# Kernel tuning notes

Hardware: AMD Instinct MI355X
Metric: run time of the kernel (lower is better)

The kernel has to match this reference:

```python
import jax, jax.numpy as jnp
import numpy as np

VOCAB = 50257   # N_max = len(word_to_idx)
IN_DIM = 256
HID = 13        # forced: out Linear in_features = 2*hidden_dim must equal dec output 2*13
L = 2048


def _lstm_dir(seq, Wih, Whh, b, reverse):
    """Single-direction LSTM over seq [T, F] with zero init. b = b_ih + b_hh.
    Torch gate order: i, f, g, o."""
    H = Whh.shape[1]

    def step(carry, x_t):
        h, c = carry
        z = Wih @ x_t + Whh @ h + b                  # (4H,)
        i, f, g, o = jnp.split(z, 4)
        c2 = jax.nn.sigmoid(f) * c + jax.nn.sigmoid(i) * jnp.tanh(g)
        h2 = jax.nn.sigmoid(o) * jnp.tanh(c2)
        return (h2, c2), h2

    init = (jnp.zeros((H,), seq.dtype), jnp.zeros((H,), seq.dtype))
    (hn, cn), hs = jax.lax.scan(step, init, seq, reverse=reverse)
    return hs, hn, cn


def _dec_cell(x_scalar, h, c, Wih, Whh, b):
    """One LSTM cell step with scalar input (input_size=1). Returns new h."""
    z = Wih[:, 0] * x_scalar + Whh @ h + b
    i, f, g, o = jnp.split(z, 4)
    c2 = jax.nn.sigmoid(f) * c + jax.nn.sigmoid(i) * jnp.tanh(g)
    return jax.nn.sigmoid(o) * jnp.tanh(c2)


def setup_inputs() -> dict:
    key = jax.random.key(0)
    ks = jax.random.split(key, 16)
    s = 0.05
    G = 4 * HID  # 52; also num_layers*2*HID = 52 (proj in_features)
    return {
        "x": jax.random.randint(ks[0], (L,), 0, VOCAB),
        "emb_W": jax.random.normal(ks[1], (VOCAB + 1, IN_DIM)) * s,
        "enc_Wih0": jax.random.normal(ks[2], (2, G, IN_DIM)) * s,   # [dir, 4H, in]
        "enc_Whh0": jax.random.normal(ks[3], (2, G, HID)) * s,
        "enc_b0": jax.random.normal(ks[4], (2, G)) * s,
        "enc_Wih1": jax.random.normal(ks[5], (2, G, 2 * HID)) * s,  # layer1 input = 2*HID
        "enc_Whh1": jax.random.normal(ks[6], (2, G, HID)) * s,
        "enc_b1": jax.random.normal(ks[7], (2, G)) * s,
        "proj1_W": jax.random.normal(ks[8], (2 * HID, 2 * 2 * HID)) * s,
        "proj1_b": jax.random.normal(ks[9], (2 * HID,)) * s,
        "proj2_W": jax.random.normal(ks[10], (2 * HID, 2 * 2 * HID)) * s,
        "proj2_b": jax.random.normal(ks[11], (2 * HID,)) * s,
        "dec_Wih": jax.random.normal(ks[12], (2, G, 1)) * s,
        "dec_Whh": jax.random.normal(ks[13], (2, G, HID)) * s,
        "dec_b": jax.random.normal(ks[14], (2, G)) * s,
        "out_W": jax.random.normal(ks[15], (VOCAB, 2 * HID)) * s,
        "out_b": jnp.zeros((VOCAB,), jnp.float32),
    }


def reference(x, emb_W, enc_Wih0, enc_Whh0, enc_b0, enc_Wih1, enc_Whh1, enc_b1,
              proj1_W, proj1_b, proj2_W, proj2_b, dec_Wih, dec_Whh, dec_b,
              out_W, out_b):
    embs = emb_W[x]                                            # (L, IN_DIM)

    # Encoder: 2-layer bidirectional LSTM, batch=1 (vectors).
    hs_f0, hnf0, cnf0 = _lstm_dir(embs, enc_Wih0[0], enc_Whh0[0], enc_b0[0], False)
    hs_b0, hnb0, cnb0 = _lstm_dir(embs, enc_Wih0[1], enc_Whh0[1], enc_b0[1], True)
    out0 = jnp.concatenate([hs_f0, hs_b0], axis=-1)            # (L, 2*HID)
    _, hnf1, cnf1 = _lstm_dir(out0, enc_Wih1[0], enc_Whh1[0], enc_b1[0], False)
    _, hnb1, cnb1 = _lstm_dir(out0, enc_Wih1[1], enc_Whh1[1], enc_b1[1], True)

    # torch h_n layout: [l0_fwd, l0_bwd, l1_fwd, l1_bwd]
    h_flat = jnp.concatenate([hnf0, hnb0, hnf1, hnb1])         # (52,)
    c_flat = jnp.concatenate([cnf0, cnb0, cnf1, cnb1])
    state_h = (proj1_W @ h_flat + proj1_b).reshape(2, HID)     # dec (dir, HID) init
    state_c = (proj2_W @ c_flat + proj2_b).reshape(2, HID)

    # Decoder step 0: input -1.0 with projected initial state.
    start = jnp.float32(-1.0)
    step0 = jnp.concatenate([
        _dec_cell(start, state_h[0], state_c[0], dec_Wih[0], dec_Whh[0], dec_b[0]),
        _dec_cell(start, state_h[1], state_c[1], dec_Wih[1], dec_Whh[1], dec_b[1]),
    ])                                                          # (26,)

    # Steps i>0: original code calls self.dec(input) with NO hidden state, so each
    # step uses zero initial state and depends only on x[i-1] -> fully parallel.
    xs = x[:-1].astype(jnp.float32)                             # (L-1,)
    z0 = jnp.zeros((HID,), jnp.float32)
    rest = jax.vmap(lambda v: jnp.concatenate([
        _dec_cell(v, z0, z0, dec_Wih[0], dec_Whh[0], dec_b[0]),
        _dec_cell(v, z0, z0, dec_Wih[1], dec_Whh[1], dec_b[1]),
    ]))(xs)                                                     # (L-1, 26)

    dec_out = jnp.concatenate([step0[None, :], rest], axis=0)   # (L, 26)
    preds = dec_out @ out_W.T + out_b                           # (L, VOCAB)
    return preds, embs
```

## Files before the change

kernel.cpp:

```cpp
#include <hip/hip_runtime.h>
#include <hip/hip_bf16.h>
#include <cstdint>
#include <cstddef>

#define L      2048
#define IN_DIM 256
#define HID    13
#define G      52
#define VOCAB  50257
#define PRED_N ((size_t)L * VOOCAB)
#define L2E    1.4426950408889634f
#define INV2L2E 0.34657359027997264f
#define NTX    99
#define NTY    16
#define NTILE  (NTX * NTY)
#define GB     254
#undef PRED_N
#define PRED_N ((size_t)L * VOCAB)

static __device__ __forceinline__ float fexp2(float x) { return __builtin_amdgcn_exp2f(x); }
static __device__ __forceinline__ float frcp(float x) { return __builtin_amdgcn_rcpf(x); }
static __device__ __forceinline__ float sigm(float z) { return 1.f - frcp(fexp2(z * L2E) + 1.f); }
static __device__ __forceinline__ float tanh_(float z) { return 1.f - 2.f * frcp(fexp2(z * (2.f * L2E)) + 1.f); }
static __device__ __forceinline__ float bcast(float v, int l) {
    return __int_as_float(__builtin_amdgcn_readlane(__float_as_int(v), l));
}

__global__ void __launch_bounds__(160) k_emb_u0(
    const int* __restrict__ x, const float* __restrict__ embW,
    const float* __restrict__ Wih0, const float* __restrict__ b0,
    const float* __restrict__ dWih, const float* __restrict__ db,
    float* __restrict__ out_embs, float* __restrict__ u0, float* __restrict__ dec)
{
    __shared__ float se[IN_DIM];
    int t = blockIdx.x;
    int tid = threadIdx.x;
    if (tid < 128) {
        int rowx = x[t];
        float2 e = ((const float2*)(embW + (size_t)rowx * IN_DIM))[tid];
        se[2 * tid]     = e.x;
        se[2 * tid + 1] = e.y;
        ((float2*)(out_embs + (size_t)t * IN_DIM))[tid] = e;
    }
    __syncthreads();
    if (tid < 2 * G) {
        int dirg = tid / G, g = tid % G;
        int gate = g / HID, row = g % HID;
        float msc = (gate == 2) ? 2.f * L2E : L2E;
        float acc = b0[dirg * G + g];
        const float* w = Wih0 + (size_t)(dirg * G + g) * IN_DIM;
        #pragma unroll 8
        for (int k = 0; k < IN_DIM; ++k)
            acc = fmaf(w[k], se[k], acc);
        u0[((size_t)dirg * L + t) * 64 + gate * 16 + row] = msc * acc;
    } else if (tid < 128) {
        int p = tid - 2 * G;
        int dirp = p / 12, pp = p % 12;
        int gate = pp / 3, row = HID + pp % 3;
        u0[((size_t)dirp * L + t) * 64 + gate * 16 + row] = 0.f;
    } else if (tid < 128 + 2 * HID && t >= 1) {
        int j = tid - 128;
        int dir = j / HID, jj = j % HID;
        float v = (float)x[t - 1];
        int base = dir * G;
        float zi = fmaf(dWih[base + jj],           v, db[base + jj]);
        float zg = fmaf(dWih[base + 2 * HID + jj], v, db[base + 2 * HID + jj]);
        float zo = fmaf(dWih[base + 3 * HID + jj], v, db[base + 3 * HID + jj]);
        float c2 = sigm(zi) * tanh_(zg);
        dec[(size_t)t * (2 * HID) + j] = sigm(zo) * tanh_(c2);
    }
}

template<bool DOUT>
static __device__ __forceinline__ void chain_run(
    const float* __restrict__ ub, int pstep,
    const float* __restrict__ whh, float kcv, float onev,
    bool m16, bool m32,
    float* __restrict__ outp,
    float& hout, float& cout)
{
    float h = 0.f, c = 0.f;
    float cur[8], nxt[8];
    #pragma unroll
    for (int k = 0; k < 8; ++k) cur[k] = ub[k * pstep];
    #pragma unroll
    for (int k = 0; k < 8; ++k) nxt[k] = cur[k];
    const float* upf = ub + (ptrdiff_t)8 * pstep;

    for (int tcb = 0; tcb < L; tcb += 8) {
        if (tcb + 8 < L) {
            #pragma unroll
            for (int k = 0; k < 8; ++k) nxt[k] = upf[k * pstep];
            upf += (ptrdiff_t)8 * pstep;
        }
        #pragma unroll
        for (int k = 0; k < 8; ++k) {
            float h0 = bcast(h, 0), h1 = bcast(h, 1), h2 = bcast(h, 2), h3 = bcast(h, 3);
            float h4 = bcast(h, 4), h5 = bcast(h, 5), h6 = bcast(h, 6), h7 = bcast(h, 7);
            float h8 = bcast(h, 8), h9 = bcast(h, 9), h10 = bcast(h, 10), h11 = bcast(h, 11);
            float h12 = bcast(h, 12);
            float A = fmaf(whh[0], h0, cur[k]);
            float B = whh[1] * h1;
            float C = whh[2] * h2;
            float D = whh[3] * h3;
            A = fmaf(whh[4], h4, A);   B = fmaf(whh[5], h5, B);
            C = fmaf(whh[6], h6, C);   D = fmaf(whh[7], h7, D);
            A = fmaf(whh[8], h8, A);   B = fmaf(whh[9], h9, B);
            C = fmaf(whh[10], h10, C); D = fmaf(whh[11], h11, D);
            A = fmaf(whh[12], h12, A);
            float z = (A + B) + (C + D);
            float act = fmaf(-kcv, frcp(fexp2(z) + 1.f), onev);
            float pa = act, pb = act;
            asm("s_nop 1\n\tv_permlane16_swap_b32 %0, %1" : "+v"(pa), "+v"(pb));
            float sf = m16 ? pa : pb;
            float qa = act, qb = act;
            asm("s_nop 1\n\tv_permlane32_swap_b32 %0, %1" : "+v"(qa), "+v"(qb));
            float tg = m32 ? qa : qb;
            float ra = tg, rb = tg;
            asm("s_nop 1\n\tv_permlane16_swap_b32 %0, %1" : "+v"(ra), "+v"(rb));
            float so = m16 ? ra : rb;
            float c2 = fmaf(sf, c, act * tg);
            float th = fmaf(-2.f, frcp(fexp2(c2) + 1.f), 1.f);
            h = so * th;
            c = c2;
            if (DOUT) { *outp = h; outp += pstep; }
        }
        #pragma unroll
        for (int k = 0; k < 8; ++k) cur[k] = nxt[k];
    }
    hout = h; cout = c;
}

static __device__ __forceinline__ void chain_setup_and_run(
    const float* __restrict__ u, const float* __restrict__ Whh,
    float* __restrict__ out0p, float* __restrict__ finh, float* __restrict__ finc,
    int chain_base, int do_out0, int dir, int lane)
{
    int lg16 = lane & 15, gate = lane >> 4;
    int rsrc = gate * HID + (lg16 < HID ? lg16 : HID - 1);
    float kcv, onev;
    if (gate == 2)      { kcv = 2.f;        onev = 1.f; }
    else if (gate == 0) { kcv = 2.f * L2E;  onev = 2.f * L2E; }
    else                { kcv = 1.f;        onev = 1.f; }
    float msc = (gate == 2) ? 2.f * L2E : L2E;
    float whh[HID];
    #pragma unroll
    for (int k = 0; k < HID; ++k) whh[k] = msc * Whh[(dir * G + rsrc) * HID + k];

    int ia = lane, ib = lane;
    asm("s_nop 1\n\tv_permlane16_swap_b32 %0, %1" : "+v"(ia), "+v"(ib));
    bool m16 = (ia == (lane ^ 16));
    int ja = lane, jb = lane;
    asm("s_nop 1\n\tv_permlane32_swap_b32 %0, %1" : "+v"(ja), "+v"(jb));
    bool m32 = (ja == (lane ^ 32));

    const float* ub = u + (size_t)dir * L * 64 + (dir ? (size_t)(L - 1) * 64 : 0) + lane;
    int pstep = dir ? -64 : 64;
    float* outp = out0p + ((size_t)dir * L + (dir ? L - 1 : 0)) * 64 + lane;

    float h, c;
    if (do_out0) chain_run<true >(ub, pstep, whh, kcv, onev, m16, m32, outp, h, c);
    else         chain_run<false>(ub, pstep, whh, kcv, onev, m16, m32, outp, h, c);

    if (lane < HID) {
        finh[(chain_base + dir) * HID + lane] = h;
        finc[(chain_base + dir) * HID + lane] = c * INV2L2E;
    }
}

__global__ void __launch_bounds__(256) k_phase0(
    const float* __restrict__ u, const float* __restrict__ Whh,
    float* __restrict__ out0p, float* __restrict__ finh, float* __restrict__ finc,
    const float* __restrict__ dec, const float* __restrict__ outW,
    const float* __restrict__ outb, float* __restrict__ preds)
{
    __shared__ float sd[128][28];
    int bid = blockIdx.x;
    int tid = threadIdx.x;
    if (bid >= 2) {
        __builtin_amdgcn_s_setprio(0);
        int b = bid - 2;
        const int q = NTILE / GB, r = NTILE % GB;
        int start = b * q + (b < r ? b : r);
        int cnt   = q + (b < r ? 1 : 0);
        for (int tt = 0; tt < cnt; ++tt) {
            int tile = start + tt;
            int ix = tile % NTX, iy = tile / NTX;
            int nbase = ix * 512, i0 = iy * 128;
            __syncthreads();
            for (int li = tid; li < 128 * 26; li += 256) {
                int rr_ = li / 26, cc = li % 26;
                sd[rr_][cc] = dec[(size_t)(i0 + rr_) * 26 + cc];
            }
            __syncthreads();
            int n0 = nbase + tid, n1 = nbase + 256 + tid;
            bool a0 = n0 < VOCAB, a1 = n1 < VOCAB;
            float w0[26], w1[26], b0v = 0.f, b1v = 0.f;
            #pragma unroll
            for (int k = 0; k < 26; ++k) { w0[k] = 0.f; w1[k] = 0.f; }
            if (a0) { const float* w = outW + (size_t)n0 * 26;
                #pragma unroll
                for (int k = 0; k < 26; ++k) w0[k] = w[k];
                b0v = outb[n0]; }
            if (a1) { const float* w = outW + (size_t)n1 * 26;
                #pragma unroll
                for (int k = 0; k < 26; ++k) w1[k] = w[k];
                b1v = outb[n1]; }
            for (int i = 0; i < 128; ++i) {
                int grow = i0 + i;
                float acc0 = b0v, acc1 = b1v;
                const float* dr = sd[i];
                #pragma unroll
                for (int k = 0; k < 26; ++k) {
                    float d = dr[k];
                    acc0 = fmaf(d, w0[k], acc0);
                    acc1 = fmaf(d, w1[k], acc1);
                }
                if (grow != 0) {
                    size_t rb = (size_t)grow * VOCAB;
                    if (a0) preds[rb + n0] = acc0;
                    if (a1) preds[rb + n1] = acc1;
                }
            }
        }
        return;
    }
    if (tid >= 64) return;
    __builtin_amdgcn_s_setprio(3);
    chain_setup_and_run(u, Whh, out0p, finh, finc, 0, 1, bid, tid);
}

__global__ void __launch_bounds__(64) k_phase1(
    const float* __restrict__ u, const float* __restrict__ Whh,
    float* __restrict__ finh, float* __restrict__ finc)
{
    chain_setup_and_run(u, Whh, (float*)nullptr, finh, finc, 2, 0, blockIdx.x, threadIdx.x);
}

__global__ void k_u1(const float* __restrict__ out0p, const float* __restrict__ Wih1,
                     const float* __restrict__ b1, float* __restrict__ u1)
{
    int idx = blockIdx.x * blockDim.x + threadIdx.x;
    if (idx >= L * 2 * 64) return;
    int t    = idx >> 7;
    int remv = idx & 127;
    int d1   = remv >> 6;
    int lane = remv & 63;
    int gate = lane >> 4, row = lane & 15;
    size_t oidx = ((size_t)d1 * L + t) * 64 + lane;
    if (row >= HID) { u1[oidx] = 0.f; return; }
    int g = gate * HID + row;
    float msc = (gate == 2) ? 2.f * L2E : L2E;
    float acc = b1[d1 * G + g];
    const float* w = Wih1 + (size_t)(d1 * G + g) * (2 * HID);
    const float* o0 = out0p + (size_t)t * 64;
    const float* o1 = out0p + ((size_t)L + t) * 64;
    #pragma unroll
    for (int k = 0; k < HID; ++k)
        acc = fmaf(w[k], o0[k], acc);
    #pragma unroll
    for (int k = 0; k < HID; ++k)
        acc = fmaf(w[HID + k], o1[k], acc);
    u1[oidx] = msc * acc;
}

__global__ void __launch_bounds__(64) k_final(const float* __restrict__ fin_h, const float* __restrict__ fin_c,
                                              const float* __restrict__ p1W, const float* __restrict__ p1b,
                                              const float* __restrict__ p2W, const float* __restrict__ p2b,
                                              const float* __restrict__ dWih, const float* __restrict__ dWhh,
                                              const float* __restrict__ db, float* __restrict__ dec)
{
    __shared__ float sh[2 * HID], sc[2 * HID], sz[G];
    int tid = threadIdx.x;
    if (tid < 4 * HID) {
        int r = tid < 2 * HID ? tid : tid - 2 * HID;
        const float* W   = tid < 2 * HID ? p1W : p2W;
        const float* src = tid < 2 * HID ? fin_h : fin_c;
        float acc = tid < 2 * HID ? p1b[r] : p2b[r];
        for (int k = 0; k < 4 * HID; ++k) acc = fmaf(W[r * 4 * HID + k], src[k], acc);
        if (tid < 2 * HID) sh[r] = acc; else sc[r] = acc;
    }
    __syncthreads();
    for (int dir = 0; dir < 2; ++dir) {
        if (tid < G) {
            float acc = db[dir * G + tid] - dWih[dir * G + tid];
            for (int k = 0; k < HID; ++k)
                acc = fmaf(dWhh[(dir * G + tid) * HID + k], sh[dir * HID + k], acc);
            sz[tid] = acc;
        }
        __syncthreads();
        if (tid < HID) {
            float si = sigm(sz[tid]);
            float sf = sigm(sz[HID + tid]);
            float tg = tanh_(sz[2 * HID + tid]);
            float so = sigm(sz[3 * HID + tid]);
            float c2 = fmaf(sf, sc[dir * HID + tid], si * tg);
            dec[dir * HID + tid] = so * tanh_(c2);
        }
        __syncthreads();
    }
}

__global__ void k_row0(const float* __restrict__ dec, const float* __restrict__ outW,
                       const float* __restrict__ outb, float* __restrict__ preds)
{
    int n = blockIdx.x * blockDim.x + threadIdx.x;
    if (n >= VOCAB) return;
    float acc = outb[n];
    const float* w = outW + (size_t)n * 26;
    #pragma unroll
    for (int k = 0; k < 26; ++k) acc = fmaf(w[k], dec[k], acc);
    preds[n] = acc;
}

extern "C" void kernel_launch(void* const* d_in, const int* in_sizes, int n_in,
                              void* d_out, int out_size, void* d_ws, size_t ws_size,
                              hipStream_t stream)
{
    (void)in_sizes; (void)n_in; (void)out_size; (void)ws_size;

    const int*   x     = (const int*)d_in[0];
    const float* embW  = (const float*)d_in[1];
    const float* eWih0 = (const float*)d_in[2];
    const float* eWhh0 = (const float*)d_in[3];
    const float* eb0   = (const float*)d_in[4];
    const float* eWih1 = (const float*)d_in[5];
    const float* eWhh1 = (const float*)d_in[6];
    const float* eb1   = (const float*)d_in[7];
    const float* p1W   = (const float*)d_in[8];
    const float* p1b   = (const float*)d_in[9];
    const float* p2W   = (const float*)d_in[10];
    const float* p2b   = (const float*)d_in[11];
    const float* dWih  = (const float*)d_in[12];
    const float* dWhh  = (const float*)d_in[13];
    const float* db    = (const float*)d_in[14];
    const float* outW  = (const float*)d_in[15];
    const float* outb  = (const float*)d_in[16];

    float* ws    = (float*)d_ws;
    float* u0    = ws;
    float* u1    = u0 + 2 * L * 64;
    float* out0p = u1 + 2 * L * 64;
    float* dec   = out0p + 2 * L * 64;
    float* fin_h = dec + L * 2 * HID;
    float* fin_c = fin_h + G;

    float* preds    = (float*)d_out;
    float* out_embs = preds + PRED_N;

    hipLaunchKernelGGL(k_emb_u0, dim3(L), dim3(160), 0, stream,
                       x, embW, eWih0, eb0, dWih, db, out_embs, u0, dec);

    hipLaunchKernelGGL(k_phase0, dim3(2 + GB), dim3(256), 0, stream,
                       u0, eWhh0, out0p, fin_h, fin_c,
                       dec, outW, outb, preds);

    hipLaunchKernelGGL(k_u1, dim3((L * 2 * 64 + 255) / 256), dim3(256), 0, stream,
                       out0p, eWih1, eb1, u1);

    hipLaunchKernelGGL(k_phase1, dim3(2), dim3(64), 0, stream,
                       u1, eWhh1, fin_h, fin_c);

    hipLaunchKernelGGL(k_final, dim3(1), dim3(64), 0, stream,
                       fin_h, fin_c, p1W, p1b, p2W, p2b, dWih, dWhh, db, dec);

    hipLaunchKernelGGL(k_row0, dim3((VOCAB + 255) / 256), dim3(256), 0, stream,
                       dec, outW, outb, preds);
}
```

Before: 576.2 us.

## Fuse embedding/u0 into phase0 with flag-based streaming to recurrent chains

Merges the embedding and layer-0 input projection kernel into the phase0 kernel. Helper blocks produce u0 in 16-step chunks and publish per-chunk release flags, which the recurrent chain blocks wait on, so the chain starts before all of u0 exists. The layer-1 input projection is fused into phase1 the same way, with per-32-step flags. The vocab output tiles are now handed out through an atomic ticket and wait only on the dec rows they read. This removes kernel-launch boundaries and overlaps the serial LSTM chains with the parallel work, at the cost of spin-wait polling, an extra memset, and a dependence on producer blocks being scheduled alongside the waiting chain blocks.

After: 764.6 us. +32.7%, slower.

```diff
diff --git a/kernel.cpp b/kernel.cpp
--- a/kernel.cpp
+++ b/kernel.cpp
@@ -8,15 +8,14 @@
 #define HID    13
 #define G      52
 #define VOCAB  50257
-#define PRED_N ((size_t)L * VOOCAB)
+#define PRED_N ((size_t)L * VOCAB)
 #define L2E    1.4426950408889634f
 #define INV2L2E 0.34657359027997264f
 #define NTX    99
-#define NTY    16
-#define NTILE  (NTX * NTY)
-#define GB     254
-#undef PRED_N
-#define PRED_N ((size_t)L * VOCAB)
+#define NTILE  (NTX * 16)
+#define NEMB   128
+#define NU1    64
+#define DYNLDS 49152
 
 static __device__ __forceinline__ float fexp2(float x) { return __builtin_amdgcn_exp2f(x); }
 static __device__ __forceinline__ float frcp(float x) { return __builtin_amdgcn_rcpf(x); }
@@ -25,116 +24,96 @@
 static __device__ __forceinline__ float bcast(float v, int l) {
     return __int_as_float(__builtin_amdgcn_readlane(__float_as_int(v), l));
 }
-
-__global__ void __launch_bounds__(160) k_emb_u0(
-    const int* __restrict__ x, const float* __restrict__ embW,
-    const float* __restrict__ Wih0, const float* __restrict__ b0,
-    const float* __restrict__ dWih, const float* __restrict__ db,
-    float* __restrict__ out_embs, float* __restrict__ u0, float* __restrict__ dec)
-{
-    __shared__ float se[IN_DIM];
-    int t = blockIdx.x;
-    int tid = threadIdx.x;
-    if (tid < 128) {
-        int rowx = x[t];
-        float2 e = ((const float2*)(embW + (size_t)rowx * IN_DIM))[tid];
-        se[2 * tid]     = e.x;
-        se[2 * tid + 1] = e.y;
-        ((float2*)(out_embs + (size_t)t * IN_DIM))[tid] = e;
-    }
-    __syncthreads();
-    if (tid < 2 * G) {
-        int dirg = tid / G, g = tid % G;
-        int gate = g / HID, row = g % HID;
-        float msc = (gate == 2) ? 2.f * L2E : L2E;
-        float acc = b0[dirg * G + g];
-        const float* w = Wih0 + (size_t)(dirg * G + g) * IN_DIM;
-        #pragma unroll 8
-        for (int k = 0; k < IN_DIM; ++k)
-            acc = fmaf(w[k], se[k], acc);
-        u0[((size_t)dirg * L + t) * 64 + gate * 16 + row] = msc * acc;
-    } else if (tid < 128) {
-        int p = tid - 2 * G;
-        int dirp = p / 12, pp = p % 12;
-        int gate = pp / 3, row = HID + pp % 3;
-        u0[((size_t)dirp * L + t) * 64 + gate * 16 + row] = 0.f;
-    } else if (tid < 128 + 2 * HID && t >= 1) {
-        int j = tid - 128;
-        int dir = j / HID, jj = j % HID;
-        float v = (float)x[t - 1];
-        int base = dir * G;
-        float zi = fmaf(dWih[base + jj],           v, db[base + jj]);
-        float zg = fmaf(dWih[base + 2 * HID + jj], v, db[base + 2 * HID + jj]);
-        float zo = fmaf(dWih[base + 3 * HID + jj], v, db[base + 3 * HID + jj]);
-        float c2 = sigm(zi) * tanh_(zg);
-        dec[(size_t)t * (2 * HID) + j] = sigm(zo) * tanh_(c2);
+static __device__ __forceinline__ void waitflag(int* f) {
+    while (__hip_atomic_load(f, __ATOMIC_ACQUIRE, __HIP_MEMORY_SCOPE_AGENT) == 0)
+        __builtin_amdgcn_s_sleep(2);
+}
+
+static __device__ __forceinline__ void compute8(
+    const float* buf, const float* whh, float kcv, float onev,
+    bool m16, bool m32, float& h, float& c, float* h8)
+{
+    #pragma unroll
+    for (int k = 0; k < 8; ++k) {
+        float h0 = bcast(h, 0), h1 = bcast(h, 1), h2 = bcast(h, 2), h3 = bcast(h, 3);
+        float h4 = bcast(h, 4), h5 = bcast(h, 5), h6 = bcast(h, 6), h7 = bcast(h, 7);
+        float h8_ = bcast(h, 8), h9 = bcast(h, 9), h10 = bcast(h, 10), h11 = bcast(h, 11);
+        float h12 = bcast(h, 12);
+        float A = fmaf(whh[0], h0, buf[k]);
+        float B = whh[1] * h1;
+        float C = whh[2] * h2;
+        float D = whh[3] * h3;
+        A = fmaf(whh[4], h4, A);   B = fmaf(whh[5], h5, B);
+        C = fmaf(whh[6], h6, C);   D = fmaf(whh[7], h7, D);
+        A = fmaf(whh[8], h8_, A);  B = fmaf(whh[9], h9, B);
+        C = fmaf(whh[10], h10, C); D = fmaf(whh[11], h11, D);
+        A = fmaf(whh[12], h12, A);
+        float z = (A + B) + (C + D);
+        float act = fmaf(-kcv, frcp(fexp2(z) + 1.f), onev);
+        float pa = act, pb = act;
+        asm("s_nop 1\n\tv_permlane16_swap_b32 %0, %1" : "+v"(pa), "+v"(pb));
+        float sf = m16 ? pa : pb;
+        float qa = act, qb = act;
+        asm("s_nop 1\n\tv_permlane32_swap_b32 %0, %1" : "+v"(qa), "+v"(qb));
+        float tg = m32 ? qa : qb;
+        float ra = tg, rb = tg;
+        asm("s_nop 1\n\tv_permlane16_swap_b32 %0, %1" : "+v"(ra), "+v"(rb));
+        float so = m16 ? ra : rb;
+        float c2 = fmaf(sf, c, act * tg);
+        float th = fmaf(-2.f, frcp(fexp2(c2) + 1.f), 1.f);
+        h = so * th;
+        c = c2;
+        h8[k] = h;
     }
 }
 
 template<bool DOUT>
-static __device__ __forceinline__ void chain_run(
-    const float* __restrict__ ub, int pstep,
-    const float* __restrict__ whh, float kcv, float onev,
-    bool m16, bool m32,
-    float* __restrict__ outp,
+static __device__ __forceinline__ void chain_core(
+    const float* ub, int pstep, const float* whh, float kcv, float onev,
+    bool m16, bool m32, float* outp, int* flg, int fcmask, int fshift, int dir,
     float& hout, float& cout)
 {
+    float bufA[8], bufB[8], h8[8];
     float h = 0.f, c = 0.f;
-    float cur[8], nxt[8];
+    waitflag(&flg[dir ? ((L - 1) >> fshift) : 0]);
     #pragma unroll
-    for (int k = 0; k < 8; ++k) cur[k] = ub[k * pstep];
+    for (int k = 0; k < 8; ++k) bufA[k] = ub[k * pstep];
     #pragma unroll
-    for (int k = 0; k < 8; ++k) nxt[k] = cur[k];
-    const float* upf = ub + (ptrdiff_t)8 * pstep;
-
-    for (int tcb = 0; tcb < L; tcb += 8) {
-        if (tcb + 8 < L) {
-            #pragma unroll
-            for (int k = 0; k < 8; ++k) nxt[k] = upf[k * pstep];
-            upf += (ptrdiff_t)8 * pstep;
-        }
-        #pragma unroll
-        for (int k = 0; k < 8; ++k) {
-            float h0 = bcast(h, 0), h1 = bcast(h, 1), h2 = bcast(h, 2), h3 = bcast(h, 3);
-            float h4 = bcast(h, 4), h5 = bcast(h, 5), h6 = bcast(h, 6), h7 = bcast(h, 7);
-            float h8 = bcast(h, 8), h9 = bcast(h, 9), h10 = bcast(h, 10), h11 = bcast(h, 11);
-            float h12 = bcast(h, 12);
-            float A = fmaf(whh[0], h0, cur[k]);
-            float B = whh[1] * h1;
-            float C = whh[2] * h2;
-            float D = whh[3] * h3;
-            A = fmaf(whh[4], h4, A);   B = fmaf(whh[5], h5, B);
-            C = fmaf(whh[6], h6, C);   D = fmaf(whh[7], h7, D);
-            A = fmaf(whh[8], h8, A);   B = fmaf(whh[9], h9, B);
-            C = fmaf(whh[10], h10, C); D = fmaf(whh[11], h11, D);
-            A = fmaf(whh[12], h12, A);
-            float z = (A + B) + (C + D);
-            float act = fmaf(-kcv, frcp(fexp2(z) + 1.f), onev);
-            float pa = act, pb = act;
-            asm("s_nop 1\n\tv_permlane16_swap_b32 %0, %1" : "+v"(pa), "+v"(pb));
-            float sf = m16 ? pa : pb;
-            float qa = act, qb = act;
-            asm("s_nop 1\n\tv_permlane32_swap_b32 %0, %1" : "+v"(qa), "+v"(qb));
-            float tg = m32 ? qa : qb;
-            float ra = tg, rb = tg;
-            asm("s_nop 1\n\tv_permlane16_swap_b32 %0, %1" : "+v"(ra), "+v"(rb));
-            float so = m16 ? ra : rb;
-            float c2 = fmaf(sf, c, act * tg);
-            float th = fmaf(-2.f, frcp(fexp2(c2) + 1.f), 1.f);
-            h = so * th;
-            c = c2;
-            if (DOUT) { *outp = h; outp += pstep; }
-        }
-        #pragma unroll
-        for (int k = 0; k < 8; ++k) cur[k] = nxt[k];
+    for (int k = 0; k < 8; ++k) bufB[k] = ub[(8 + k) * pstep];
+
+    for (int tcb = 0; tcb < L; tcb += 16) {
+        compute8(bufA, whh, kcv, onev, m16, m32, h, c, h8);
+        if (DOUT) {
+            #pragma unroll
+            for (int k = 0; k < 8; ++k) outp[k * pstep] = h8[k];
+            outp += 8 * pstep;
+        }
+        if (tcb + 16 < L) {
+            int tp = tcb + 16;
+            if ((tp & fcmask) == 0) waitflag(&flg[(dir ? (L - 1 - tp) : tp) >> fshift]);
+            #pragma unroll
+            for (int k = 0; k < 8; ++k) bufA[k] = ub[(tp + k) * pstep];
+        }
+        compute8(bufB, whh, kcv, onev, m16, m32, h, c, h8);
+        if (DOUT) {
+            #pragma unroll
+            for (int k = 0; k < 8; ++k) outp[k * pstep] = h8[k];
+            outp += 8 * pstep;
+        }
+        if (tcb + 24 < L) {
+            int tp = tcb + 24;
+            #pragma unroll
+            for (int k = 0; k < 8; ++k) bufB[k] = ub[(tp + k) * pstep];
+        }
     }
     hout = h; cout = c;
 }
 
-static __device__ __forceinline__ void chain_setup_and_run(
-    const float* __restrict__ u, const float* __restrict__ Whh,
-    float* __restrict__ out0p, float* __restrict__ finh, float* __restrict__ finc,
-    int chain_base, int do_out0, int dir, int lane)
+template<bool DOUT>
+static __device__ __forceinline__ void run_chain(
+    const float* u, const float* Whh, float* out0p,
+    float* finh, float* finc, int chain_base,
+    int* flg, int fcmask, int fshift, int dir, int lane)
 {
     int lg16 = lane & 15, gate = lane >> 4;
     int rsrc = gate * HID + (lg16 < HID ? lg16 : HID - 1);
@@ -156,11 +135,10 @@
 
     const float* ub = u + (size_t)dir * L * 64 + (dir ? (size_t)(L - 1) * 64 : 0) + lane;
     int pstep = dir ? -64 : 64;
-    float* outp = out0p + ((size_t)dir * L + (dir ? L - 1 : 0)) * 64 + lane;
+    float* outp = out0p ? out0p + ((size_t)dir * L + (dir ? L - 1 : 0)) * 64 + lane : (float*)nullptr;
 
     float h, c;
-    if (do_out0) chain_run<true >(ub, pstep, whh, kcv, onev, m16, m32, outp, h, c);
-    else         chain_run<false>(ub, pstep, whh, kcv, onev, m16, m32, outp, h, c);
+    chain_core<DOUT>(ub, pstep, whh, kcv, onev, m16, m32, outp, flg, fcmask, fshift, dir, h, c);
 
     if (lane < HID) {
         finh[(chain_base + dir) * HID + lane] = h;
@@ -169,99 +147,174 @@
 }
 
 __global__ void __launch_bounds__(256) k_phase0(
-    const float* __restrict__ u, const float* __restrict__ Whh,
-    float* __restrict__ out0p, float* __restrict__ finh, float* __restrict__ finc,
-    const float* __restrict__ dec, const float* __restrict__ outW,
-    const float* __restrict__ outb, float* __restrict__ preds)
-{
-    __shared__ float sd[128][28];
-    int bid = blockIdx.x;
-    int tid = threadIdx.x;
-    if (bid >= 2) {
-        __builtin_amdgcn_s_setprio(0);
-        int b = bid - 2;
-        const int q = NTILE / GB, r = NTILE % GB;
-        int start = b * q + (b < r ? b : r);
-        int cnt   = q + (b < r ? 1 : 0);
-        for (int tt = 0; tt < cnt; ++tt) {
-            int tile = start + tt;
-            int ix = tile % NTX, iy = tile / NTX;
-            int nbase = ix * 512, i0 = iy * 128;
+    const int* __restrict__ x, const float* __restrict__ embW,
+    const float* __restrict__ Wih0, const float* __restrict__ b0,
+    const float* __restrict__ dWih, const float* __restrict__ db,
+    const float* __restrict__ Whh0,
+    const float* __restrict__ outW, const float* __restrict__ outb,
+    float* __restrict__ u0, float* __restrict__ out0p, float* __restrict__ dec,
+    float* __restrict__ out_embs, float* __restrict__ preds,
+    float* __restrict__ finh, float* __restrict__ finc,
+    int* __restrict__ flags0, int* __restrict__ ticket)
+{
+    extern __shared__ float dynls[];
+    __shared__ int s_tk;
+    int bid = blockIdx.x, tid = threadIdx.x;
+
+    if (bid < 2) {
+        if (tid >= 64) return;
+        __builtin_amdgcn_s_setprio(3);
+        run_chain<true>(u0, Whh0, out0p, finh, finc, 0, flags0, 15, 4, bid, tid);
+        return;
+    }
+
+    if (bid - 2 < NEMB) {
+        int t0 = (bid - 2) * 16;
+        for (int j = 0; j < 8; ++j) {
+            int t = t0 + 2 * j;
+            {
+                int rr = tid >> 7, cc = tid & 127;
+                int tt = t + rr;
+                int rowx = x[tt];
+                float2 e = ((const float2*)(embW + (size_t)rowx * IN_DIM))[cc];
+                dynls[rr * IN_DIM + 2 * cc]     = e.x;
+                dynls[rr * IN_DIM + 2 * cc + 1] = e.y;
+                ((float2*)(out_embs + (size_t)tt * IN_DIM))[cc] = e;
+            }
             __syncthreads();
-            for (int li = tid; li < 128 * 26; li += 256) {
-                int rr_ = li / 26, cc = li % 26;
-                sd[rr_][cc] = dec[(size_t)(i0 + rr_) * 26 + cc];
+            if (tid < 208) {
+                int tt = t + (tid >= 104);
+                int q = tid % 104;
+                int dirg = q / G, g = q % G;
+                int gate = g / HID, row = g % HID;
+                float msc = (gate == 2) ? 2.f * L2E : L2E;
+                float acc = b0[dirg * G + g];
+                const float* w  = Wih0 + (size_t)(dirg * G + g) * IN_DIM;
+                const float* se = dynls + (tid >= 104 ? IN_DIM : 0);
+                #pragma unroll 8
+                for (int k = 0; k < IN_DIM; ++k) acc = fmaf(w[k], se[k], acc);
+                u0[((size_t)dirg * L + tt) * 64 + gate * 16 + row] = msc * acc;
+            } else {
+                int p = tid - 208;
+                int tt = t + (p >= 24);
+                int pp = p % 24;
+                int dirp = pp / 12, r = pp % 12;
+                u0[((size_t)dirp * L + tt) * 64 + (r / 3) * 16 + 13 + r % 3] = 0.f;
+            }
+            if (tid < 52) {
+                int tt = t + (tid >= 26);
+                if (tt >= 1) {
+                    int j2 = tid % 26;
+                    int dir = j2 / HID, jj = j2 % HID;
+                    float v = (float)x[tt - 1];
+                    int base = dir * G;
+                    float zi = fmaf(dWih[base + jj],           v, db[base + jj]);
+                    float zg = fmaf(dWih[base + 2 * HID + jj], v, db[base + 2 * HID + jj]);
+                    float zo = fmaf(dWih[base + 3 * HID + jj], v, db[base + 3 * HID + jj]);
+                    float c2 = sigm(zi) * tanh_(zg);
+                    dec[(size_t)tt * (2 * HID) + j2] = sigm(zo) * tanh_(c2);
+                }
             }
             __syncthreads();
-            int n0 = nbase + tid, n1 = nbase + 256 + tid;
-            bool a0 = n0 < VOCAB, a1 = n1 < VOCAB;
-            float w0[26], w1[26], b0v = 0.f, b1v = 0.f;
-            #pragma unroll
-            for (int k = 0; k < 26; ++k) { w0[k] = 0.f; w1[k] = 0.f; }
-            if (a0) { const float* w = outW + (size_t)n0 * 26;
+        }
+        __syncthreads();
+        __threadfence();
+        if (tid == 0)
+            __hip_atomic_store(&flags0[bid - 2], 1, __ATOMIC_RELEASE, __HIP_MEMORY_SCOPE_AGENT);
+    }
+
+    float* sd = dynls;
+    for (;;) {
+        __syncthreads();
+        if (tid == 0) s_tk = atomicAdd(ticket, 1);
+        __syncthreads();
+        int tile = s_tk;
+        if (tile >= NTILE) return;
+        int ix = tile % NTX, iy = tile / NTX;
+        int nbase = ix * 512, i0 = iy * 128;
+        if (tid < 8) waitflag(&flags0[iy * 8 + tid]);
+        __syncthreads();
+        for (int li = tid; li < 128 * 26; li += 256) {
+            int rr = li / 26, cc = li % 26;
+            sd[rr * 28 + cc] = dec[(size_t)(i0 + rr) * 26 + cc];
+        }
+        __syncthreads();
+        int n0 = nbase + tid, n1 = nbase + 256 + tid;
+        bool a0 = n0 < VOCAB, a1 = n1 < VOCAB;
+        float w0[26], w1[26], b0v = 0.f, b1v = 0.f;
+        #pragma unroll
+        for (int k = 0; k < 26; ++k) { w0[k] = 0.f; w1[k] = 0.f; }
+        if (a0) { const float* w = outW + (size_t)n0 * 26;
+            #pragma unroll
+            for (int k = 0; k < 26; ++k) w0[k] = w[k];
+            b0v = outb[n0]; }
+        if (a1) { const float* w = outW + (size_t)n1 * 26;
+            #pragma unroll
+            for (int k = 0; k < 26; ++k) w1[k] = w[k];
+            b1v = outb[n1]; }
+        for (int i = 0; i < 128; ++i) {
+            int grow = i0 + i;
+            float acc0 = b0v, acc1 = b1v;
+            const float* dr = sd + i * 28;
+            #pragma unroll
+            for (int k = 0; k < 26; ++k) {
+                float d = dr[k];
+                acc0 = fmaf(d, w0[k], acc0);
+                acc1 = fmaf(d, w1[k], acc1);
+            }
+            if (grow != 0) {
+                size_t rb = (size_t)grow * VOCAB;
+                if (a0) preds[rb + n0] = acc0;
+                if (a1) preds[rb + n1] = acc1;
+            }
+        }
+    }
+}
+
+__global__ void __launch_bounds__(256) k_phase1(
+    const float* __restrict__ out0p, const float* __restrict__ Wih1,
+    const float* __restrict__ b1, const float* __restrict__ Whh1,
+    float* __restrict__ u1, float* __restrict__ finh, float* __restrict__ finc,
+    int* __restrict__ flags1)
+{
+    extern __shared__ float dynls[];
+    int bid = blockIdx.x, tid = threadIdx.x;
+    if (bid < 2) {
+        if (tid >= 64) return;
+        __builtin_amdgcn_s_setprio(3);
+        run_chain<false>(u1, Whh1, (float*)nullptr, finh, finc, 2, flags1, 31, 5, bid, tid);
+        return;
+    }
+    if (bid - 2 >= NU1) return;
+    int t0 = (bid - 2) * 32;
+    for (int j = 0; j < 32; ++j) {
+        int t = t0 + j;
+        if (tid < 26) {
+            int src = tid < 13 ? t : (L + t);
+            dynls[tid] = out0p[(size_t)src * 64 + (tid % 13)];
+        }
+        __syncthreads();
+        if (tid < 128) {
+            int d1 = tid >> 6, lane = tid & 63;
+            int gate = lane >> 4, row = lane & 15;
+            size_t oidx = ((size_t)d1 * L + t) * 64 + lane;
+            if (row < HID) {
+                int g = gate * HID + row;
+                float msc = (gate == 2) ? 2.f * L2E : L2E;
+                float acc = b1[d1 * G + g];
+                const float* w = Wih1 + (size_t)(d1 * G + g) * (2 * HID);
                 #pragma unroll
-                for (int k = 0; k < 26; ++k) w0[k] = w[k];
-                b0v = outb[n0]; }
-            if (a1) { const float* w = outW + (size_t)n1 * 26;
-                #pragma unroll
-                for (int k = 0; k < 26; ++k) w1[k] = w[k];
-                b1v = outb[n1]; }
-            for (int i = 0; i < 128; ++i) {
-                int grow = i0 + i;
-                float acc0 = b0v, acc1 = b1v;
-                const float* dr = sd[i];
-                #pragma unroll
-                for (int k = 0; k < 26; ++k) {
-                    float d = dr[k];
-                    acc0 = fmaf(d, w0[k], acc0);
-                    acc1 = fmaf(d, w1[k], acc1);
-                }
-                if (grow != 0) {
-                    size_t rb = (size_t)grow * VOCAB;
-                    if (a0) preds[rb + n0] = acc0;
-                    if (a1) preds[rb + n1] = acc1;
-                }
-            }
-        }
-        return;
-    }
-    if (tid >= 64) return;
-    __builtin_amdgcn_s_setprio(3);
-    chain_setup_and_run(u, Whh, out0p, finh, finc, 0, 1, bid, tid);
-}
-
-__global__ void __launch_bounds__(64) k_phase1(
-    const float* __restrict__ u, const float* __restrict__ Whh,
-    float* __restrict__ finh, float* __restrict__ finc)
-{
-    chain_setup_and_run(u, Whh, (float*)nullptr, finh, finc, 2, 0, blockIdx.x, threadIdx.x);
-}
-
-__global__ void k_u1(const float* __restrict__ out0p, const float* __restrict__ Wih1,
-                     const float* __restrict__ b1, float* __restrict__ u1)
-{
-    int idx = blockIdx.x * blockDim.x + threadIdx.x;
-    if (idx >= L * 2 * 64) return;
-    int t    = idx >> 7;
-    int remv = idx & 127;
-    int d1   = remv >> 6;
-    int lane = remv & 63;
-    int gate = lane >> 4, row = lane & 15;
-    size_t oidx = ((size_t)d1 * L + t) * 64 + lane;
-    if (row >= HID) { u1[oidx] = 0.f; return; }
-    int g = gate * HID + row;
-    float msc = (gate == 2) ? 2.f * L2E : L2E;
-    float acc = b1[d1 * G + g];
-    const float* w = Wih1 + (size_t)(d1 * G + g) * (2 * HID);
-    const float* o0 = out0p + (size_t)t * 64;
-    const float* o1 = out0p + ((size_t)L + t) * 64;
-    #pragma unroll
-    for (int k = 0; k < HID; ++k)
-        acc = fmaf(w[k], o0[k], acc);
-    #pragma unroll
-    for (int k = 0; k < HID; ++k)
-        acc = fmaf(w[HID + k], o1[k], acc);
-    u1[oidx] = msc * acc;
+                for (int k = 0; k < 2 * HID; ++k) acc = fmaf(w[k], dynls[k], acc);
+                u1[oidx] = msc * acc;
+            } else {
+                u1[oidx] = 0.f;
+            }
+        }
+        __syncthreads();
+    }
+    __threadfence();
+    if (tid == 0)
+        __hip_atomic_store(&flags1[bid - 2], 1, __ATOMIC_RELEASE, __HIP_MEMORY_SCOPE_AGENT);
 }
 
 __global__ void __launch_bounds__(64) k_final(const float* __restrict__ fin_h, const float* __restrict__ fin_c,
@@ -343,23 +396,23 @@
     float* out0p = u1 + 2 * L * 64;
     float* dec   = out0p + 2 * L * 64;
     float* fin_h = dec + L * 2 * HID;
-    float* fin_c = fin_h + G;
+    float* fin_c = fin_h + 64;
+    int*   ctrl  = (int*)(fin_c + 64);
+    int*   flags0 = ctrl;
+    int*   flags1 = ctrl + 128;
+    int*   ticket = ctrl + 192;
 
     float* preds    = (float*)d_out;
     float* out_embs = preds + PRED_N;
 
-    hipLaunchKernelGGL(k_emb_u0, dim3(L), dim3(160), 0, stream,
-                       x, embW, eWih0, eb0, dWih, db, out_embs, u0, dec);
-
-    hipLaunchKernelGGL(k_phase0, dim3(2 + GB), dim3(256), 0, stream,
-                       u0, eWhh0, out0p, fin_h, fin_c,
-                       dec, outW, outb, preds);
-
-    hipLaunchKernelGGL(k_u1, dim3((L * 2 * 64 + 255) / 256), dim3(256), 0, stream,
-                       out0p, eWih1, eb1, u1);
-
-    hipLaunchKernelGGL(k_phase1, dim3(2), dim3(64), 0, stream,
-                       u1, eWhh1, fin_h, fin_c);
+    hipMemsetAsync(ctrl, 0, 193 * sizeof(int), stream);
+
+    hipLaunchKernelGGL(k_phase0, dim3(256), dim3(256), DYNLDS, stream,
+                       x, embW, eWih0, eb0, dWih, db, eWhh0, outW, outb,
+                       u0, out0p, dec, out_embs, preds, fin_h, fin_c, flags0, ticket);
+
+    hipLaunchKernelGGL(k_phase1, dim3(256), dim3(256), DYNLDS, stream,
+                       out0p, eWih1, eb1, eWhh1, u1, fin_h, fin_c, flags1);
 
     hipLaunchKernelGGL(k_final, dim3(1), dim3(64), 0, stream,
                        fin_h, fin_c, p1W, p1b, p2W, p2b, dWih, dWhh, db, dec);
```
